# Optimization experiments

Hardware: AMD Instinct MI355X
Metric: run time of the kernel (lower is better)

The kernel has to match this reference:

```python
import jax, jax.numpy as jnp
import numpy as np


def setup_inputs() -> dict:
    key = jax.random.key(0)
    k1, k2, k3, k4, k5 = jax.random.split(key, 5)
    B, S, ENC, DEC = 32, 2048, 1024, 512
    hidden = jax.random.normal(k1, (B, DEC), dtype=jnp.float32)
    encoder_outputs = jax.random.normal(k2, (B, S, ENC), dtype=jnp.float32)
    W = jax.random.normal(k3, (DEC, ENC + DEC), dtype=jnp.float32) * (1.0 / np.sqrt(ENC + DEC))
    b = jax.random.normal(k4, (DEC,), dtype=jnp.float32) * 0.01
    v = jax.random.uniform(k5, (DEC,), dtype=jnp.float32)  # torch.rand init
    return {"hidden": hidden, "encoder_outputs": encoder_outputs, "W": W, "b": b, "v": v}


def reference(hidden, encoder_outputs, W, b, v):
    # hidden: [B, D_dec], encoder_outputs: [B, S, D_enc]
    # Concat order in original: (hidden, encoder_outputs) -> split W accordingly.
    D_dec = hidden.shape[-1]
    Wh = W[:, :D_dec]   # [D_dec, D_dec] acts on hidden
    We = W[:, D_dec:]   # [D_dec, D_enc] acts on encoder_outputs
    # energy: tanh(Linear(cat(hidden_repeated, enc))) == tanh(h@Wh^T + enc@We^T + b)
    h_proj = jnp.einsum('bd,ed->be', hidden, Wh)                 # [B, D_dec]
    e_proj = jnp.einsum('bse,de->bsd', encoder_outputs, We)      # [B, S, D_dec]
    energy = jnp.tanh(e_proj + h_proj[:, None, :] + b)           # [B, S, D_dec]
    # scores: v . energy per (b, s); softmax over src_len
    scores = jnp.einsum('d,bsd->bs', v, energy)                  # [B, S]
    attn = jax.nn.softmax(scores, axis=-1)
    return attn[:, None, :]                                       # [B, 1, S]
```

## Files before the change

### kernel.cpp

```cpp
#include <hip/hip_runtime.h>
#include <hip/hip_bf16.h>


typedef __attribute__((ext_vector_type(8))) short bf16x8;
typedef __attribute__((ext_vector_type(4))) float f32x4;

__device__ __forceinline__ ushort f2bf(float x) {
    __hip_bfloat16 h = __float2bfloat16(x);
    return *reinterpret_cast<ushort*>(&h);
}

__device__ __forceinline__ ushort4 pack4(float4 a) {
    ushort4 o;
    o.x = f2bf(a.x); o.y = f2bf(a.y); o.z = f2bf(a.z); o.w = f2bf(a.w);
    return o;
}

#define WS_WBF   0
#define WS_HB    (1u << 20)
#define WS_SCORE ((1u << 20) + (64u << 10))

__global__ void prep_kernel(const float* __restrict__ W,
                            const float* __restrict__ hidden,
                            const float* __restrict__ bias,
                            ushort* __restrict__ Wbf,
                            float* __restrict__ hb) {
    const int bid = blockIdx.x, tid = threadIdx.x;
    if (bid < 512) {
        int idx = bid * 256 + tid;
        int d  = idx >> 8;
        int e4 = (idx & 255) * 4;
        float4 f = *(const float4*)(W + (size_t)d * 1536 + 512 + e4);
        ushort4 u;
        u.x = f2bf(f.x); u.y = f2bf(f.y); u.z = f2bf(f.z); u.w = f2bf(f.w);
        *(ushort4*)(Wbf + (size_t)d * 1024 + e4) = u;
    } else {
        int idx = (bid - 512) * 256 + tid;
        int b = idx >> 9, d = idx & 511;
        const float4* hp = (const float4*)(hidden + b * 512);
        const float4* wp = (const float4*)(W + (size_t)d * 1536);
        float acc = 0.f;
#pragma unroll 8
        for (int j = 0; j < 128; ++j) {
            float4 h = hp[j], w = wp[j];
            acc += h.x * w.x + h.y * w.y + h.z * w.z + h.w * w.w;
        }
        hb[idx] = acc + bias[d];
    }
}

__launch_bounds__(512, 2)
__global__ void eproj_scores(const float* __restrict__ enc,
                             const ushort* __restrict__ Wbf,
                             const float* __restrict__ hb,
                             const float* __restrict__ v,
                             float* __restrict__ scores) {
    __shared__ alignas(16) ushort Abuf[4][2048];

    const int tid  = threadIdx.x;
    const int lane = tid & 63, w = tid >> 6;
    const int q = lane >> 4, ln = lane & 15;
    const long m0   = (long)blockIdx.x * 64;
    const int  bidx = (int)(m0 >> 11);
    const int  n0   = w * 64;

    f32x4 acc[4][4];
#pragma unroll
    for (int mt = 0; mt < 4; ++mt)
#pragma unroll
        for (int nt = 0; nt < 4; ++nt)
            acc[mt][nt] = (f32x4){0.f, 0.f, 0.f, 0.f};

    const ushort* bptr[4];
#pragma unroll
    for (int nt = 0; nt < 4; ++nt)
        bptr[nt] = Wbf + (size_t)(n0 + nt * 16 + ln) * 1024 + q * 8;

    const int sr = tid >> 3, sq = tid & 7;
    const float* aptr = enc + (m0 + sr) * 1024 + sq * 4;
    const int awoff = sr * 32 + (((sq >> 1) ^ (sr & 3)) << 3) + (sq & 1) * 4;

    int rdoff[4];
#pragma unroll
    for (int mt = 0; mt < 4; ++mt) {
        int rA = mt * 16 + ln;
        rdoff[mt] = rA * 32 + ((q ^ (rA & 3)) << 3);
    }

    float4 ar[2];
    ar[0] = *(const float4*)(aptr);
    ar[1] = *(const float4*)(aptr + 32);

    bf16x8 bfr[2][4];
#pragma unroll
    for (int nt = 0; nt < 4; ++nt)
        bfr[0][nt] = *(const bf16x8*)(bptr[nt]);

    *(ushort4*)(&Abuf[0][awoff]) = pack4(ar[0]);
    ar[0] = *(const float4*)(aptr + 64);

    for (int g = 0; g < 8; ++g) {
#pragma unroll
        for (int j = 0; j < 4; ++j) {
            const int kt = g * 4 + j;
            const int p  = (j + 1) & 1;
            if (kt + 1 < 32) {
                *(ushort4*)(&Abuf[(j + 1) & 3][awoff]) = pack4(ar[p]);
                if (kt + 3 < 32)
                    ar[p] = *(const float4*)(aptr + (kt + 3) * 32);
                asm volatile("s_waitcnt lgkmcnt(0)" ::: "memory");
            }
            __builtin_amdgcn_s_barrier();
            asm volatile("" ::: "memory");

            if (kt + 1 < 32) {
#pragma unroll
                for (int nt = 0; nt < 4; ++nt)
                    bfr[p][nt] = *(const bf16x8*)(bptr[nt] + (size_t)(kt + 1) * 32);
            }
#pragma unroll
            for (int mt = 0; mt < 4; ++mt) {
                bf16x8 af = *(const bf16x8*)(&Abuf[j][rdoff[mt]]);
#pragma unroll
                for (int nt = 0; nt < 4; ++nt)
                    acc[mt][nt] = __builtin_amdgcn_mfma_f32_16x16x32_bf16(
                        af, bfr[j & 1][nt], acc[mt][nt], 0, 0, 0);
            }
        }
    }

    float partial[4][4];
#pragma unroll
    for (int mt = 0; mt < 4; ++mt)
#pragma unroll
        for (int r = 0; r < 4; ++r) partial[mt][r] = 0.f;

#pragma unroll
    for (int nt = 0; nt < 4; ++nt) {
        int d = n0 + nt * 16 + ln;
        float hbv = hb[bidx * 512 + d];
        float vv  = v[d];
#pragma unroll
        for (int mt = 0; mt < 4; ++mt)
#pragma unroll
            for (int r = 0; r < 4; ++r) {
                float x = acc[mt][nt][r] + hbv;
                float e = __expf(2.f * x);
                partial[mt][r] += vv * (1.f - 2.f / (e + 1.f));
            }
    }
#pragma unroll
    for (int mt = 0; mt < 4; ++mt)
#pragma unroll
        for (int r = 0; r < 4; ++r) {
            float s = partial[mt][r];
            s += __shfl_xor(s, 1);
            s += __shfl_xor(s, 2);
            s += __shfl_xor(s, 4);
            s += __shfl_xor(s, 8);
            partial[mt][r] = s;
        }

    __syncthreads();
    float* spart = (float*)Abuf;
    if (ln == 0) {
#pragma unroll
        for (int mt = 0; mt < 4; ++mt)
#pragma unroll
            for (int r = 0; r < 4; ++r)
                spart[w * 64 + mt * 16 + q * 4 + r] = partial[mt][r];
    }
    __syncthreads();
    if (tid < 64) {
        float s = 0.f;
#pragma unroll
        for (int ww = 0; ww < 8; ++ww) s += spart[ww * 64 + tid];
        scores[m0 + tid] = s;
    }
}

__global__ void softmax_kernel(const float* __restrict__ scores, float* __restrict__ out) {
    int b = blockIdx.x;
    const float* sc = scores + b * 2048;
    __shared__ float wred[4], wsum[4];

    float lmax = -1e30f;
    for (int i = threadIdx.x; i < 2048; i += 256) lmax = fmaxf(lmax, sc[i]);
#pragma unroll
    for (int m = 1; m < 64; m <<= 1) lmax = fmaxf(lmax, __shfl_xor(lmax, m));
    if ((threadIdx.x & 63) == 0) wred[threadIdx.x >> 6] = lmax;
    __syncthreads();
    float gmax = fmaxf(fmaxf(wred[0], wred[1]), fmaxf(wred[2], wred[3]));

    float lsum = 0.f;
    for (int i = threadIdx.x; i < 2048; i += 256) lsum += __expf(sc[i] - gmax);
#pragma unroll
    for (int m = 1; m < 64; m <<= 1) lsum += __shfl_xor(lsum, m);
    if ((threadIdx.x & 63) == 0) wsum[threadIdx.x >> 6] = lsum;
    __syncthreads();
    float inv = 1.f / (wsum[0] + wsum[1] + wsum[2] + wsum[3]);

    for (int i = threadIdx.x; i < 2048; i += 256)
        out[b * 2048 + i] = __expf(sc[i] - gmax) * inv;
}

extern "C" void kernel_launch(void* const* d_in, const int* in_sizes, int n_in,
                              void* d_out, int out_size, void* d_ws, size_t ws_size,
                              hipStream_t stream) {
    const float* hidden = (const float*)d_in[0];
    const float* enc    = (const float*)d_in[1];
    const float* W      = (const float*)d_in[2];
    const float* bias   = (const float*)d_in[3];
    const float* v      = (const float*)d_in[4];
    float* out = (float*)d_out;

    char* ws = (char*)d_ws;
    ushort* Wbf   = (ushort*)(ws + WS_WBF);
    float*  hb    = (float*)(ws + WS_HB);
    float*  score = (float*)(ws + WS_SCORE);

    hipLaunchKernelGGL(prep_kernel,  dim3(576),  dim3(256), 0, stream,
                       W, hidden, bias, Wbf, hb);
    hipLaunchKernelGGL(eproj_scores, dim3(1024), dim3(512), 0, stream,
                       enc, Wbf, hb, v, score);
    hipLaunchKernelGGL(softmax_kernel, dim3(32), dim3(256), 0, stream, score, out);
}
```

Before: 513.5 us.

## Stream encoder tiles into LDS with direct global-to-LDS loads, double-buffered

Replaces the register-staged fp32 load, bf16 pack and LDS store pipeline with global_load_lds DMA of fp32 encoder windows (256 columns by 64 rows) into a double-buffered 128 KB dynamic LDS area with XOR swizzle. Conversion to bf16 now happens after the LDS read, just before each MFMA. Barriers drop from one per k-step to two per window. The intent is to cut VGPR staging and per-step synchronisation. In exchange it uses 128 KB of LDS, which likely allows only one 512-thread block per CU despite launch_bounds(512,2), and it doubles the LDS bytes read.

```diff
diff --git a/kernel.cpp b/kernel.cpp
--- a/kernel.cpp
+++ b/kernel.cpp
@@ -10,9 +10,12 @@
     return *reinterpret_cast<ushort*>(&h);
 }
 
-__device__ __forceinline__ ushort4 pack4(float4 a) {
-    ushort4 o;
-    o.x = f2bf(a.x); o.y = f2bf(a.y); o.z = f2bf(a.z); o.w = f2bf(a.w);
+__device__ __forceinline__ bf16x8 pack8(float4 a, float4 b) {
+    bf16x8 o;
+    o[0] = (short)f2bf(a.x); o[1] = (short)f2bf(a.y);
+    o[2] = (short)f2bf(a.z); o[3] = (short)f2bf(a.w);
+    o[4] = (short)f2bf(b.x); o[5] = (short)f2bf(b.y);
+    o[6] = (short)f2bf(b.z); o[7] = (short)f2bf(b.w);
     return o;
 }
 
@@ -55,7 +58,7 @@
                              const float* __restrict__ hb,
                              const float* __restrict__ v,
                              float* __restrict__ scores) {
-    __shared__ alignas(16) ushort Abuf[4][2048];
+    extern __shared__ float Abuf[];
 
     const int tid  = threadIdx.x;
     const int lane = tid & 63, w = tid >> 6;
@@ -76,57 +79,68 @@
     for (int nt = 0; nt < 4; ++nt)
         bptr[nt] = Wbf + (size_t)(n0 + nt * 16 + ln) * 1024 + q * 8;
 
-    const int sr = tid >> 3, sq = tid & 7;
-    const float* aptr = enc + (m0 + sr) * 1024 + sq * 4;
-    const int awoff = sr * 32 + (((sq >> 1) ^ (sr & 3)) << 3) + (sq & 1) * 4;
-
-    int rdoff[4];
-#pragma unroll
-    for (int mt = 0; mt < 4; ++mt) {
-        int rA = mt * 16 + ln;
-        rdoff[mt] = rA * 32 + ((q ^ (rA & 3)) << 3);
-    }
-
-    float4 ar[2];
-    ar[0] = *(const float4*)(aptr);
-    ar[1] = *(const float4*)(aptr + 32);
-
+    auto dma_window = [&](int wi) {
+        float* base = Abuf + (size_t)(wi & 1) * 16384;
+#pragma unroll
+        for (int i = 0; i < 8; ++i) {
+            int s = i * 512 + tid;
+            int r = s >> 6, c = s & 63;
+            int cg = c ^ (r & 7);
+            const float* g = enc + (m0 + r) * 1024 + wi * 256 + cg * 4;
+            float* lb = base + (size_t)s * 4;
+            __builtin_amdgcn_global_load_lds(
+                (const __attribute__((address_space(1))) void*)g,
+                (__attribute__((address_space(3))) void*)lb, 16, 0, 0);
+        }
+    };
+
+    dma_window(0);
+    dma_window(1);
     bf16x8 bfr[2][4];
 #pragma unroll
     for (int nt = 0; nt < 4; ++nt)
         bfr[0][nt] = *(const bf16x8*)(bptr[nt]);
 
-    *(ushort4*)(&Abuf[0][awoff]) = pack4(ar[0]);
-    ar[0] = *(const float4*)(aptr + 64);
-
-    for (int g = 0; g < 8; ++g) {
-#pragma unroll
-        for (int j = 0; j < 4; ++j) {
-            const int kt = g * 4 + j;
-            const int p  = (j + 1) & 1;
-            if (kt + 1 < 32) {
-                *(ushort4*)(&Abuf[(j + 1) & 3][awoff]) = pack4(ar[p]);
-                if (kt + 3 < 32)
-                    ar[p] = *(const float4*)(aptr + (kt + 3) * 32);
-                asm volatile("s_waitcnt lgkmcnt(0)" ::: "memory");
+    int rA[4], rx[4];
+#pragma unroll
+    for (int mt = 0; mt < 4; ++mt) {
+        rA[mt] = mt * 16 + ln;
+        rx[mt] = rA[mt] & 7;
+    }
+
+    for (int wi = 0; wi < 4; ++wi) {
+        if (wi < 3) asm volatile("s_waitcnt vmcnt(8)" ::: "memory");
+        else        asm volatile("s_waitcnt vmcnt(0)" ::: "memory");
+        __builtin_amdgcn_s_barrier();
+        asm volatile("" ::: "memory");
+
+        const float* AW = Abuf + (size_t)(wi & 1) * 16384;
+#pragma unroll
+        for (int j = 0; j < 8; ++j) {
+            const int kt = wi * 8 + j;
+            if (wi < 3 || j < 7) {
+#pragma unroll
+                for (int nt = 0; nt < 4; ++nt)
+                    bfr[(j + 1) & 1][nt] =
+                        *(const bf16x8*)(bptr[nt] + (size_t)(kt + 1) * 32);
             }
-            __builtin_amdgcn_s_barrier();
-            asm volatile("" ::: "memory");
-
-            if (kt + 1 < 32) {
-#pragma unroll
-                for (int nt = 0; nt < 4; ++nt)
-                    bfr[p][nt] = *(const bf16x8*)(bptr[nt] + (size_t)(kt + 1) * 32);
-            }
 #pragma unroll
             for (int mt = 0; mt < 4; ++mt) {
-                bf16x8 af = *(const bf16x8*)(&Abuf[j][rdoff[mt]]);
+                const float* Ar = AW + rA[mt] * 256;
+                int c0 = j * 8 + q * 2;
+                float4 a0 = *(const float4*)(Ar + ((c0    ) ^ rx[mt]) * 4);
+                float4 a1 = *(const float4*)(Ar + ((c0 + 1) ^ rx[mt]) * 4);
+                bf16x8 af = pack8(a0, a1);
 #pragma unroll
                 for (int nt = 0; nt < 4; ++nt)
                     acc[mt][nt] = __builtin_amdgcn_mfma_f32_16x16x32_bf16(
                         af, bfr[j & 1][nt], acc[mt][nt], 0, 0, 0);
             }
         }
+
+        __builtin_amdgcn_s_barrier();
+        asm volatile("" ::: "memory");
+        if (wi + 2 < 4) dma_window(wi + 2);
     }
 
     float partial[4][4];
@@ -162,7 +176,7 @@
         }
 
     __syncthreads();
-    float* spart = (float*)Abuf;
+    float* spart = Abuf;
     if (ln == 0) {
 #pragma unroll
         for (int mt = 0; mt < 4; ++mt)
@@ -221,7 +235,7 @@
 
     hipLaunchKernelGGL(prep_kernel,  dim3(576),  dim3(256), 0, stream,
                        W, hidden, bias, Wbf, hb);
-    hipLaunchKernelGGL(eproj_scores, dim3(1024), dim3(512), 0, stream,
+    hipLaunchKernelGGL(eproj_scores, dim3(1024), dim3(512), 131072, stream,
                        enc, Wbf, hb, v, score);
     hipLaunchKernelGGL(softmax_kernel, dim3(32), dim3(256), 0, stream, score, out);
 }
```

After: 529.3 us. 1.03x slower.
